# Optimization experiments

Hardware: AMD Instinct MI355X
Metric: run time of the kernel (lower is better)

## Reference

```python
import math
import jax, jax.numpy as jnp
import numpy as np

B, N, M = 8, 1024, 32
D = 128      # node_dim
E = 32       # edge_dim
DD = 32      # dist_dim
MSG = 128    # message_dim
P = 128      # proj_dim
THETA = 10000.0


def _linear(x, w, b):
    return x @ w + b


def _sinusoidal(t, dim, theta=THETA):
    half = dim // 2
    freqs = jnp.exp(jnp.arange(half, dtype=t.dtype) * (-math.log(theta) / (half - 1)))
    ang = t[..., None] * freqs  # (..., half)
    return jnp.concatenate([jnp.sin(ang), jnp.cos(ang)], axis=-1)


def setup_inputs() -> dict:
    key = jax.random.key(0)
    ks = jax.random.split(key, 20)
    pair_in = 2 * D + E + DD  # NUM_ATOMS == 1

    def w(k, shape):
        fan_in = shape[0]
        return jax.random.uniform(k, shape, jnp.float32, -1, 1) / np.sqrt(fan_in)

    return {
        "embeddings": jax.random.normal(ks[0], (B, N, D), jnp.float32),
        "coords": jax.random.normal(ks[1], (B, N, 3), jnp.float32),
        "padding_mask": jnp.ones((B, N), jnp.float32),
        "edges": jax.random.normal(ks[2], (B, N, M, E), jnp.float32),
        "we_w1": w(ks[3], (pair_in, MSG)), "we_b1": jnp.zeros((MSG,), jnp.float32),
        "we_w2": w(ks[4], (MSG, MSG)),    "we_b2": jnp.zeros((MSG,), jnp.float32),
        "wx_w1": w(ks[5], (MSG, P)),      "wx_b1": jnp.zeros((P,), jnp.float32),
        "wx_w2": w(ks[6], (P, 1)),        "wx_b2": jnp.zeros((1,), jnp.float32),
        "wh_w1": w(ks[7], (D + MSG, P)),  "wh_b1": jnp.zeros((P,), jnp.float32),
        "wh_w2": w(ks[8], (P, D)),        "wh_b2": jnp.zeros((D,), jnp.float32),
        "neighbor_ids": jax.random.randint(ks[9], (B, N, M), 0, N),
    }


def _gather(x, idx):
    # x: (B, N, d), idx: (B, N, M) -> (B, N, M, d). Direct gather,
    # mathematically identical to the one-hot einsum in the original.
    Bx, Nx, d = x.shape
    flat = jnp.take_along_axis(x, idx.reshape(Bx, -1, 1), axis=1)
    return flat.reshape(Bx, Nx, idx.shape[-1], d)


def reference(embeddings, coords, padding_mask, edges,
              we_w1, we_b1, we_w2, we_b2,
              wx_w1, wx_b1, wx_w2, wx_b2,
              wh_w1, wh_b1, wh_w2, wh_b2,
              neighbor_ids):
    feats2 = _gather(embeddings, neighbor_ids)          # (B,N,M,D)
    n_coords = _gather(coords, neighbor_ids)            # (B,N,M,3)
    rel_coors = coords[:, :, None, :] - n_coords        # (B,N,M,3)
    rel_dist = jnp.linalg.norm(rel_coors, axis=-1)      # (B,N,M)
    dists = _sinusoidal(rel_dist, DD)                   # (B,N,M,DD)

    feats1 = jnp.broadcast_to(embeddings[:, :, None, :], feats2.shape)
    feats_pair = jnp.concatenate([feats1, feats2, dists, edges], axis=-1)

    h = jax.nn.relu(_linear(feats_pair, we_w1, we_b1))
    m_ij = _linear(h, we_w2, we_b2)                     # (B,N,M,MSG)

    # coordinate update (unit vectors are detached in the original)
    unit = jax.lax.stop_gradient(
        jnp.nan_to_num(rel_coors / rel_dist[..., None]))
    px = _linear(jax.nn.relu(_linear(m_ij, wx_w1, wx_b1)), wx_w2, wx_b2)
    coords_out = coords + (unit * px).sum(axis=2) / M

    # feature update
    m_masked = m_ij * padding_mask[:, :, None, None]
    m_i = m_masked.sum(axis=2) / M                      # (B,N,MSG)
    hh = jnp.concatenate([embeddings, m_i], axis=-1)
    ph = _linear(jax.nn.relu(_linear(hh, wh_w1, wh_b1)), wh_w2, wh_b2)
    embeddings_out = embeddings + ph

    return embeddings_out, coords_out
```

## Files before the change

kernel.cpp:

```cpp
#include <hip/hip_runtime.h>
#include <hip/hip_bf16.h>

typedef __hip_bfloat16 bf16;
typedef short short8 __attribute__((ext_vector_type(8)));
typedef float f32x4 __attribute__((ext_vector_type(4)));
typedef int   int4v __attribute__((ext_vector_type(4)));

#define NB 8
#define NN 1024
#define NM 32
#define ND 128
#define NE 32
#define NODES (NB*NN)
#define NPB 4
#define NR  (NPB*NM)

#define OFF_W1AT   0
#define OFF_W1BT   32768
#define OFF_W1CDT  65536
#define OFF_W2T    81920
#define OFF_WX1T   114688
#define OFF_WH1AT  147456
#define OFF_WH1BT  180224
#define OFF_WH2T   212992
#define OFF_Y1     245760
#define OFF_Y2     (OFF_Y1 + 2097152)
#define NEED_FAST  ((size_t)OFF_Y2 + 2097152)

__device__ __forceinline__ float toF(bf16 x){ return __bfloat162float(x); }
__device__ __forceinline__ bf16  toB(float x){ return __float2bfloat16(x); }

__device__ __forceinline__ void bar_lds(){
  asm volatile("s_waitcnt lgkmcnt(0)" ::: "memory");
  __builtin_amdgcn_s_barrier();
}

__device__ __forceinline__ short8 pin8(short8 w){
  union { short8 s; int4v i; } u; u.s = w;
  asm volatile("" : "+v"(u.i));
  return u.s;
}

__device__ __forceinline__ void cp16f(bf16* d, const float* s){
  #pragma unroll
  for (int q = 0; q < 4; ++q){
    float4 a = ((const float4*)s)[q];
    d[q*4+0]=toB(a.x); d[q*4+1]=toB(a.y); d[q*4+2]=toB(a.z); d[q*4+3]=toB(a.w);
  }
}
__device__ __forceinline__ void cp8f(bf16* d, const float* s){
  #pragma unroll
  for (int q = 0; q < 2; ++q){
    float4 a = ((const float4*)s)[q];
    d[q*4+0]=toB(a.x); d[q*4+1]=toB(a.y); d[q*4+2]=toB(a.z); d[q*4+3]=toB(a.w);
  }
}
__device__ __forceinline__ void cp4f(bf16* d, const float* s){
  float4 a = *(const float4*)s;
  d[0]=toB(a.x); d[1]=toB(a.y); d[2]=toB(a.z); d[3]=toB(a.w);
}

#define MFMA(a,b,c) __builtin_amdgcn_mfma_f32_16x16x32_bf16((a),(b),(c),0,0,0)

__global__ __launch_bounds__(256) void k_tr(const float* __restrict__ w1,
    const float* __restrict__ w2, const float* __restrict__ wx1,
    const float* __restrict__ wh1, const float* __restrict__ wh2,
    char* __restrict__ ws){
  int i = blockIdx.x*256 + threadIdx.x;
  const float* src; int koff, KT, dst, e;
  if      (i <  16384){ src=w1;  koff=0;   KT=128; dst=OFF_W1AT;  e=i; }
  else if (i <  32768){ src=w1;  koff=128; KT=128; dst=OFF_W1BT;  e=i-16384; }
  else if (i <  40960){ src=w1;  koff=256; KT=64;  dst=OFF_W1CDT; e=i-32768; }
  else if (i <  57344){ src=w2;  koff=0;   KT=128; dst=OFF_W2T;   e=i-40960; }
  else if (i <  73728){ src=wx1; koff=0;   KT=128; dst=OFF_WX1T;  e=i-57344; }
  else if (i <  90112){ src=wh1; koff=0;   KT=128; dst=OFF_WH1AT; e=i-73728; }
  else if (i < 106496){ src=wh1; koff=128; KT=128; dst=OFF_WH1BT; e=i-90112; }
  else if (i < 122880){ src=wh2; koff=0;   KT=128; dst=OFF_WH2T;  e=i-106496; }
  else return;
  int c = e / KT, k = e - c*KT;
  ((bf16*)(ws+dst))[e] = toB(src[(size_t)(koff+k)*128 + c]);
}

__global__ __launch_bounds__(256) void k_prep(const float* __restrict__ emb,
    const float* __restrict__ eb1, char* __restrict__ ws){
  __shared__ __align__(16) bf16 sE[32][136];
  const int tid = threadIdx.x, g0 = blockIdx.x*32;
  { const int row = tid >> 3, sub = tid & 7;
    cp16f(&sE[row][sub*16], emb + (size_t)(g0+row)*ND + sub*16); }
  bar_lds();
  const int lane = tid & 63, wv = tid >> 6, lr = lane & 15, lk = lane >> 4;
  const int c0 = wv*16 + lr, c1 = (wv+4)*16 + lr;
  const short* wt[2] = {(const short*)(ws+OFF_W1AT), (const short*)(ws+OFF_W1BT)};
  bf16* yo[2] = {(bf16*)(ws+OFF_Y1), (bf16*)(ws+OFF_Y2)};
  #pragma unroll
  for (int t = 0; t < 2; ++t){
    f32x4 acc[2][2] = {};
    #pragma unroll
    for (int kc = 0; kc < 4; ++kc){
      const int k0 = kc*32 + lk*8;
      short8 a0 = *(const short8*)&sE[lr][k0];
      short8 a1 = *(const short8*)&sE[16+lr][k0];
      short8 w0 = *(const short8*)&wt[t][c0*128 + k0];
      short8 w1v= *(const short8*)&wt[t][c1*128 + k0];
      acc[0][0]=MFMA(a0,w0,acc[0][0]);  acc[1][0]=MFMA(a1,w0,acc[1][0]);
      acc[0][1]=MFMA(a0,w1v,acc[0][1]); acc[1][1]=MFMA(a1,w1v,acc[1][1]);
    }
    const float b0 = (t==0) ? eb1[c0] : 0.f;
    const float b1 = (t==0) ? eb1[c1] : 0.f;
    #pragma unroll
    for (int rt = 0; rt < 2; ++rt)
      #pragma unroll
      for (int r = 0; r < 4; ++r){
        const int orow = rt*16 + lk*4 + r;
        const size_t g = (size_t)(g0 + orow)*ND;
        yo[t][g + c0] = toB(acc[rt][0][r] + b0);
        yo[t][g + c1] = toB(acc[rt][1][r] + b1);
      }
  }
}

__global__ __launch_bounds__(512) void k_edges_fast(
    const float* __restrict__ coords, const float* __restrict__ mask,
    const float* __restrict__ edges,  const float* __restrict__ eb2,
    const float* __restrict__ xb1,    const float* __restrict__ xw2,
    const float* __restrict__ xb2,    const int* __restrict__ nids,
    const char* __restrict__ ws,      float* __restrict__ out)
{
  const short* w1cdT = (const short*)(ws+OFF_W1CDT);
  const short* w2T   = (const short*)(ws+OFF_W2T);
  const short* wx1T  = (const short*)(ws+OFF_WX1T);
  const bf16*  Y1    = (const bf16*)(ws+OFF_Y1);
  const bf16*  Y2    = (const bf16*)(ws+OFF_Y2);

  __shared__ __align__(16) char regA[NR*136*2];
  __shared__ __align__(16) bf16 sH[NR][136];
  __shared__ float sUnit[NR][3];
  __shared__ float sPx[NR];
  bf16 (*sDE)[72]  = (bf16(*)[72])regA;
  bf16 (*sM)[136]  = (bf16(*)[136])regA;

  const int bid = blockIdx.x;
  const int nbk = ((bid & 7) << 8) + (bid >> 3);
  const int g0  = nbk * NPB;
  const int bi  = g0 >> 10;
  const int tid = threadIdx.x;
  const int lane = tid & 63, wv = tid >> 6;
  const int lr = lane & 15, lk = lane >> 4;
  const int c0 = wv*16 + lr;

  short8 rw1[2], rw2[4], rwx[4];
  #pragma unroll
  for (int kc = 0; kc < 2; ++kc)
    rw1[kc] = pin8(*(const short8*)&w1cdT[c0*64 + kc*32 + lk*8]);
  #pragma unroll
  for (int kc = 0; kc < 4; ++kc){
    rw2[kc] = pin8(*(const short8*)&w2T[c0*128 + kc*32 + lk*8]);
    rwx[kc] = pin8(*(const short8*)&wx1T[c0*128 + kc*32 + lk*8]);
  }
  const float b2   = eb2[c0];
  const float bx   = xb1[c0];
  const float wx2c = xw2[c0];
  const float bx2v = xb2[0];
  float mv[NPB];
  #pragma unroll
  for (int n = 0; n < NPB; ++n) mv[n] = mask[g0+n];

  {
    const int row = tid >> 2, sub = tid & 3;
    const int node = row >> 5;
    const int j = nids[(size_t)(g0+node)*NM + (row & 31)];
    const float* cs = coords + (size_t)(g0+node)*3;
    const float* cj = coords + ((size_t)bi*NN + j)*3;
    const float rx = cs[0]-cj[0], ry = cs[1]-cj[1], rz = cs[2]-cj[2];
    const float d2 = rx*rx + ry*ry + rz*rz;
    const float dist = sqrtf(d2);
    if (sub == 0){
      const float inv = (d2 > 0.f) ? 1.f/dist : 0.f;
      sUnit[row][0]=rx*inv; sUnit[row][1]=ry*inv; sUnit[row][2]=rz*inv;
    }
    cp8f(&sDE[row][32 + sub*8],
         edges + ((size_t)(g0+node)*NM + (row&31))*NE + sub*8);
    #pragma unroll
    for (int q = 0; q < 8; ++q){
      const int dd = sub*8 + q, h = dd & 15;
      const float ang = dist * __expf(-0.6140226909f * (float)h);
      sDE[row][dd] = toB((dd < 16) ? __sinf(ang) : __cosf(ang));
    }
    const bf16* y1p = Y1 + (size_t)(g0+node)*ND + sub*32;
    const bf16* y2p = Y2 + ((size_t)bi*NN + j)*ND + sub*32;
    #pragma unroll
    for (int h8 = 0; h8 < 4; ++h8){
      short8 a = *(const short8*)(y1p + h8*8);
      short8 b = *(const short8*)(y2p + h8*8);
      short8 o;
      #pragma unroll
      for (int q = 0; q < 8; ++q){
        bf16 ba, bb; short sa = a[q], sb = b[q];
        __builtin_memcpy(&ba,&sa,2); __builtin_memcpy(&bb,&sb,2);
        bf16 rsum = toB(toF(ba) + toF(bb));
        short sr; __builtin_memcpy(&sr,&rsum,2);
        o[q] = sr;
      }
      *(short8*)&sH[row][sub*32 + h8*8] = o;
    }
  }
  bar_lds();

  {
    #pragma unroll
    for (int t = 0; t < 8; ++t){
      f32x4 acc = {};
      #pragma unroll
      for (int kc = 0; kc < 2; ++kc){
        short8 a = *(const short8*)&sDE[t*16 + lr][kc*32 + lk*8];
        acc = MFMA(a, rw1[kc], acc);
      }
      #pragma unroll
      for (int r = 0; r < 4; ++r){
        const int orow = t*16 + lk*4 + r;
        sH[orow][c0] = toB(fmaxf(toF(sH[orow][c0]) + acc[r], 0.f));
      }
    }
  }
  bar_lds();

  {
    float msum[NPB] = {};
    #pragma unroll
    for (int t = 0; t < 8; ++t){
      f32x4 acc = {};
      #pragma unroll
      for (int kc = 0; kc < 4; ++kc){
        short8 a = *(const short8*)&sH[t*16 + lr][kc*32 + lk*8];
        acc = MFMA(a, rw2[kc], acc);
      }
      #pragma unroll
      for (int r = 0; r < 4; ++r){
        const int orow = t*16 + lk*4 + r;
        const float m = acc[r] + b2;
        sM[orow][c0] = toB(m);
        msum[t>>1] += m;
      }
    }
    #pragma unroll
    for (int n = 0; n < NPB; ++n){
      msum[n] += __shfl_xor(msum[n], 16);
      msum[n] += __shfl_xor(msum[n], 32);
    }
    if (lk == 0){
      #pragma unroll
      for (int n = 0; n < NPB; ++n)
        out[(size_t)(g0+n)*ND + c0] = msum[n] * mv[n] * (1.f/32.f);
    }
  }
  bar_lds();

  {
    #pragma unroll
    for (int t = 0; t < 8; ++t){
      f32x4 acc = {};
      #pragma unroll
      for (int kc = 0; kc < 4; ++kc){
        short8 a = *(const short8*)&sM[t*16 + lr][kc*32 + lk*8];
        acc = MFMA(a, rwx[kc], acc);
      }
      #pragma unroll
      for (int r = 0; r < 4; ++r){
        const int orow = t*16 + lk*4 + r;
        sH[orow][c0] = toB(fmaxf(acc[r] + bx, 0.f) * wx2c);
      }
    }
  }
  bar_lds();

  {
    const int row = tid >> 2, sub = tid & 3;
    float p = 0.f;
    #pragma unroll
    for (int c8 = 0; c8 < 4; ++c8){
      short8 x = *(const short8*)&sH[row][sub*32 + c8*8];
      #pragma unroll
      for (int q = 0; q < 8; ++q){
        bf16 bq; short sq = x[q]; __builtin_memcpy(&bq,&sq,2);
        p += toF(bq);
      }
    }
    p += __shfl_xor(p, 1); p += __shfl_xor(p, 2);
    if (sub == 0) sPx[row] = p + bx2v;
  }
  bar_lds();

  if (tid < NR){
    const float px = sPx[tid];
    float v0 = sUnit[tid][0]*px, v1 = sUnit[tid][1]*px, v2 = sUnit[tid][2]*px;
    #pragma unroll
    for (int m = 1; m < 32; m <<= 1){
      v0 += __shfl_xor(v0, m);
      v1 += __shfl_xor(v1, m);
      v2 += __shfl_xor(v2, m);
    }
    const int node = tid >> 5, d = tid & 31;
    if (d < 3){
      const float s = (d==0) ? v0 : (d==1 ? v1 : v2);
      out[(size_t)NODES*ND + (size_t)(g0+node)*3 + d] =
          coords[(size_t)(g0+node)*3 + d] + s*(1.f/32.f);
    }
  }
}

__global__ __launch_bounds__(256) void k_edges_compact(
    const float* __restrict__ emb,   const float* __restrict__ coords,
    const float* __restrict__ mask,  const float* __restrict__ edges,
    const float* __restrict__ eb1,   const float* __restrict__ eb2,
    const float* __restrict__ xb1,   const float* __restrict__ xw2,
    const float* __restrict__ xb2,   const int* __restrict__ nids,
    const char* __restrict__ ws,     float* __restrict__ out)
{
  const short* w1aT  = (const short*)(ws+OFF_W1AT);
  const short* w1bT  = (const short*)(ws+OFF_W1BT);
  const short* w1cdT = (const short*)(ws+OFF_W1CDT);
  const short* w2T   = (const short*)(ws+OFF_W2T);
  const short* wx1T  = (const short*)(ws+OFF_WX1T);

  __shared__ __align__(16) bf16 sA[32][336];
  __shared__ __align__(16) bf16 sH[32][136];
  __shared__ __align__(16) bf16 sM[32][136];
  __shared__ float sUnit[32][3];
  __shared__ float sPx[32];
  __shared__ int   sIds[32];
  __shared__ float sSelfC[3];

  const int tid = threadIdx.x;
  const int nb  = blockIdx.x;
  const int bi  = nb >> 10;

  if (tid < 32) sIds[tid] = nids[nb*NM + tid];
  if (tid < 3)  sSelfC[tid] = coords[(size_t)nb*3 + tid];
  __syncthreads();

  {
    const int row = tid >> 3, sub = tid & 7;
    const int j = sIds[row];
    cp16f(&sA[row][sub*16],       emb + (size_t)nb*ND + sub*16);
    cp16f(&sA[row][128 + sub*16], emb + ((size_t)bi*NN + j)*ND + sub*16);
    cp4f (&sA[row][288 + sub*4],  edges + ((size_t)nb*NM + row)*NE + sub*4);
    float jx = coords[((size_t)bi*NN + j)*3 + 0];
    float jy = coords[((size_t)bi*NN + j)*3 + 1];
    float jz = coords[((size_t)bi*NN + j)*3 + 2];
    float rx = sSelfC[0]-jx, ry = sSelfC[1]-jy, rz = sSelfC[2]-jz;
    float d2 = rx*rx + ry*ry + rz*rz;
    float dist = sqrtf(d2);
    if (sub == 0){
      float inv = (d2 > 0.f) ? 1.f/dist : 0.f;
      sUnit[row][0]=rx*inv; sUnit[row][1]=ry*inv; sUnit[row][2]=rz*inv;
    }
    #pragma unroll
    for (int q = 0; q < 4; ++q){
      const int dd = sub*4 + q, h = dd & 15;
      float ang = dist * __expf(-0.6140226909f * (float)h);
      sA[row][256+dd] = toB((dd < 16) ? __sinf(ang) : __cosf(ang));
    }
  }
  __syncthreads();

  const int lane = tid & 63, wv = tid >> 6, lr = lane & 15, lk = lane >> 4;
  const int c0 = wv*16 + lr, c1 = (wv+4)*16 + lr;

  {
    f32x4 acc[2][2] = {};
    #pragma unroll
    for (int kc = 0; kc < 10; ++kc){
      const int k0 = kc*32 + lk*8;
      const short* wp; int kk, KT;
      if (kc < 4){ wp = w1aT; kk = k0; KT = 128; }
      else if (kc < 8){ wp = w1bT; kk = k0-128; KT = 128; }
      else { wp = w1cdT; kk = k0-256; KT = 64; }
      short8 a0 = *(const short8*)&sA[lr][k0];
      short8 a1 = *(const short8*)&sA[16+lr][k0];
      short8 w0 = *(const short8*)&wp[c0*KT + kk];
      short8 w1v= *(const short8*)&wp[c1*KT + kk];
      acc[0][0]=MFMA(a0,w0,acc[0][0]);  acc[1][0]=MFMA(a1,w0,acc[1][0]);
      acc[0][1]=MFMA(a0,w1v,acc[0][1]); acc[1][1]=MFMA(a1,w1v,acc[1][1]);
    }
    const float b0 = eb1[c0], b1 = eb1[c1];
    #pragma unroll
    for (int rt = 0; rt < 2; ++rt)
      #pragma unroll
      for (int r = 0; r < 4; ++r){
        const int orow = rt*16 + lk*4 + r;
        sH[orow][c0] = toB(fmaxf(acc[rt][0][r]+b0, 0.f));
        sH[orow][c1] = toB(fmaxf(acc[rt][1][r]+b1, 0.f));
      }
  }
  __syncthreads();

  {
    f32x4 acc[2][2] = {};
    #pragma unroll
    for (int kc = 0; kc < 4; ++kc){
      const int k0 = kc*32 + lk*8;
      short8 a0 = *(const short8*)&sH[lr][k0];
      short8 a1 = *(const short8*)&sH[16+lr][k0];
      short8 w0 = *(const short8*)&w2T[c0*128 + k0];
      short8 w1v= *(const short8*)&w2T[c1*128 + k0];
      acc[0][0]=MFMA(a0,w0,acc[0][0]);  acc[1][0]=MFMA(a1,w0,acc[1][0]);
      acc[0][1]=MFMA(a0,w1v,acc[0][1]); acc[1][1]=MFMA(a1,w1v,acc[1][1]);
    }
    const float b0 = eb2[c0], b1 = eb2[c1];
    #pragma unroll
    for (int rt = 0; rt < 2; ++rt)
      #pragma unroll
      for (int r = 0; r < 4; ++r){
        const int orow = rt*16 + lk*4 + r;
        sM[orow][c0] = toB(acc[rt][0][r] + b0);
        sM[orow][c1] = toB(acc[rt][1][r] + b1);
      }
  }
  __syncthreads();

  {
    f32x4 acc[2][2] = {};
    #pragma unroll
    for (int kc = 0; kc < 4; ++kc){
      const int k0 = kc*32 + lk*8;
      short8 a0 = *(const short8*)&sM[lr][k0];
      short8 a1 = *(const short8*)&sM[16+lr][k0];
      short8 w0 = *(const short8*)&wx1T[c0*128 + k0];
      short8 w1v= *(const short8*)&wx1T[c1*128 + k0];
      acc[0][0]=MFMA(a0,w0,acc[0][0]);  acc[1][0]=MFMA(a1,w0,acc[1][0]);
      acc[0][1]=MFMA(a0,w1v,acc[0][1]); acc[1][1]=MFMA(a1,w1v,acc[1][1]);
    }
    const float b0 = xb1[c0], b1 = xb1[c1];
    #pragma unroll
    for (int rt = 0; rt < 2; ++rt)
      #pragma unroll
      for (int r = 0; r < 4; ++r){
        const int orow = rt*16 + lk*4 + r;
        sH[orow][c0] = toB(fmaxf(acc[rt][0][r]+b0, 0.f));
        sH[orow][c1] = toB(fmaxf(acc[rt][1][r]+b1, 0.f));
      }
  }
  __syncthreads();

  {
    const int row = tid >> 3, sub = tid & 7;
    float p = 0.f;
    #pragma unroll
    for (int q = 0; q < 16; ++q){
      const int c = sub*16 + q;
      p += toF(sH[row][c]) * xw2[c];
    }
    p += __shfl_down(p,4,8); p += __shfl_down(p,2,8); p += __shfl_down(p,1,8);
    if (sub == 0) sPx[row] = p + xb2[0];
  }
  if (tid < 128){
    float s = 0.f;
    #pragma unroll
    for (int m = 0; m < 32; ++m) s += toF(sM[m][tid]);
    out[(size_t)nb*ND + tid] = s * mask[nb] * (1.f/32.f);
  }
  __syncthreads();
  if (tid < 3){
    float s = 0.f;
    #pragma unroll
    for (int m = 0; m < 32; ++m) s += sUnit[m][tid]*sPx[m];
    out[(size_t)NODES*ND + (size_t)nb*3 + tid] = sSelfC[tid] + s*(1.f/32.f);
  }
}

__global__ __launch_bounds__(256) void k_node(
    const float* __restrict__ emb, const float* __restrict__ hb1,
    const float* __restrict__ hb2, const char* __restrict__ ws,
    float* __restrict__ out)
{
  const short* whaT = (const short*)(ws+OFF_WH1AT);
  const short* whbT = (const short*)(ws+OFF_WH1BT);
  const short* wh2T = (const short*)(ws+OFF_WH2T);
  __shared__ __align__(16) bf16 sE[32][136];
  __shared__ __align__(16) bf16 sM[32][136];
  __shared__ __align__(16) bf16 sH[32][136];
  const int tid = threadIdx.x, g0 = blockIdx.x*32;
  const int lane = tid & 63, wv = tid >> 6, lr = lane & 15, lk = lane >> 4;
  const int c0 = wv*16 + lr, c1 = (wv+4)*16 + lr;

  short8 rwa[2][4], rwb[2][4], rw2[2][4];
  #pragma unroll
  for (int kc = 0; kc < 4; ++kc){
    rwa[0][kc] = *(const short8*)&whaT[c0*128 + kc*32 + lk*8];
    rwa[1][kc] = *(const short8*)&whaT[c1*128 + kc*32 + lk*8];
    rwb[0][kc] = *(const short8*)&whbT[c0*128 + kc*32 + lk*8];
    rwb[1][kc] = *(const short8*)&whbT[c1*128 + kc*32 + lk*8];
    rw2[0][kc] = *(const short8*)&wh2T[c0*128 + kc*32 + lk*8];
    rw2[1][kc] = *(const short8*)&wh2T[c1*128 + kc*32 + lk*8];
  }
  const float b1c0 = hb1[c0], b1c1 = hb1[c1];
  const float b2c0 = hb2[c0], b2c1 = hb2[c1];

  { const int row = tid >> 3, sub = tid & 7;
    cp16f(&sE[row][sub*16], emb + (size_t)(g0+row)*ND + sub*16);
    cp16f(&sM[row][sub*16], out + (size_t)(g0+row)*ND + sub*16); }
  bar_lds();
  {
    f32x4 acc[2][2] = {};
    #pragma unroll
    for (int kc = 0; kc < 4; ++kc){
      const int k0 = kc*32 + lk*8;
      short8 a0 = *(const short8*)&sE[lr][k0];
      short8 a1 = *(const short8*)&sE[16+lr][k0];
      acc[0][0]=MFMA(a0,rwa[0][kc],acc[0][0]); acc[1][0]=MFMA(a1,rwa[0][kc],acc[1][0]);
      acc[0][1]=MFMA(a0,rwa[1][kc],acc[0][1]); acc[1][1]=MFMA(a1,rwa[1][kc],acc[1][1]);
    }
    #pragma unroll
    for (int kc = 0; kc < 4; ++kc){
      const int k0 = kc*32 + lk*8;
      short8 a0 = *(const short8*)&sM[lr][k0];
      short8 a1 = *(const short8*)&sM[16+lr][k0];
      acc[0][0]=MFMA(a0,rwb[0][kc],acc[0][0]); acc[1][0]=MFMA(a1,rwb[0][kc],acc[1][0]);
      acc[0][1]=MFMA(a0,rwb[1][kc],acc[0][1]); acc[1][1]=MFMA(a1,rwb[1][kc],acc[1][1]);
    }
    #pragma unroll
    for (int rt = 0; rt < 2; ++rt)
      #pragma unroll
      for (int r = 0; r < 4; ++r){
        const int orow = rt*16 + lk*4 + r;
        sH[orow][c0] = toB(fmaxf(acc[rt][0][r] + b1c0, 0.f));
        sH[orow][c1] = toB(fmaxf(acc[rt][1][r] + b1c1, 0.f));
      }
  }
  bar_lds();
  {
    f32x4 acc[2][2] = {};
    #pragma unroll
    for (int kc = 0; kc < 4; ++kc){
      const int k0 = kc*32 + lk*8;
      short8 a0 = *(const short8*)&sH[lr][k0];
      short8 a1 = *(const short8*)&sH[16+lr][k0];
      acc[0][0]=MFMA(a0,rw2[0][kc],acc[0][0]); acc[1][0]=MFMA(a1,rw2[0][kc],acc[1][0]);
      acc[0][1]=MFMA(a0,rw2[1][kc],acc[0][1]); acc[1][1]=MFMA(a1,rw2[1][kc],acc[1][1]);
    }
    #pragma unroll
    for (int rt = 0; rt < 2; ++rt)
      #pragma unroll
      for (int r = 0; r < 4; ++r){
        const int orow = rt*16 + lk*4 + r;
        const size_t g = (size_t)(g0 + orow)*ND;
        out[g + c0] = acc[rt][0][r] + b2c0 + emb[g + c0];
        out[g + c1] = acc[rt][1][r] + b2c1 + emb[g + c1];
      }
  }
}

extern "C" void kernel_launch(void* const* d_in, const int* in_sizes, int n_in,
                              void* d_out, int out_size, void* d_ws, size_t ws_size,
                              hipStream_t stream) {
  const float* emb    = (const float*)d_in[0];
  const float* coords = (const float*)d_in[1];
  const float* mask   = (const float*)d_in[2];
  const float* edges  = (const float*)d_in[3];
  const float* we_w1  = (const float*)d_in[4];
  const float* we_b1  = (const float*)d_in[5];
  const float* we_w2  = (const float*)d_in[6];
  const float* we_b2  = (const float*)d_in[7];
  const float* wx_w1  = (const float*)d_in[8];
  const float* wx_b1  = (const float*)d_in[9];
  const float* wx_w2  = (const float*)d_in[10];
  const float* wx_b2  = (const float*)d_in[11];
  const float* wh_w1  = (const float*)d_in[12];
  const float* wh_b1  = (const float*)d_in[13];
  const float* wh_w2  = (const float*)d_in[14];
  const float* wh_b2  = (const float*)d_in[15];
  const int*   nids   = (const int*)d_in[16];
  float* out = (float*)d_out;
  char* ws = (char*)d_ws;
  const bool fast = (ws_size >= NEED_FAST);

  k_tr<<<480,256,0,stream>>>(we_w1, we_w2, wx_w1, wh_w1, wh_w2, ws);

  if (fast){
    k_prep<<<NODES/32,256,0,stream>>>(emb, we_b1, ws);
    k_edges_fast<<<NODES/NPB,512,0,stream>>>(coords, mask, edges, we_b2,
        wx_b1, wx_w2, wx_b2, nids, ws, out);
  } else {
    k_edges_compact<<<NODES,256,0,stream>>>(emb, coords, mask, edges,
        we_b1, we_b2, wx_b1, wx_w2, wx_b2, nids, ws, out);
  }

  k_node<<<NODES/32,256,0,stream>>>(emb, wh_b1, wh_b2, ws, out);
}
```

Measured before the change: 72.43 us.

## Fold second edge linear layer into downstream weights to skip one edge GEMM

Precomputes W2·Wx1 and W2·Wh1b (plus folded biases) in a new compose kernel, so the edge kernel goes straight from the hidden activation h to the coordinate-MLP preactivation and writes the mean of h instead of m. The node kernel then uses the composed weight and adds a mask-scaled folded bias. This removes one 128x128 MFMA GEMM per edge tile, one LDS round trip and one barrier. In exchange it adds a small serial compose launch and changes the bf16 rounding points.

```diff
diff --git a/kernel.cpp b/kernel.cpp
--- a/kernel.cpp
+++ b/kernel.cpp
@@ -23,7 +23,11 @@
 #define OFF_WH1AT  147456
 #define OFF_WH1BT  180224
 #define OFF_WH2T   212992
-#define OFF_Y1     245760
+#define OFF_W2XT   245760
+#define OFF_W2HT   278528
+#define OFF_B2X    311296
+#define OFF_B2H    311808
+#define OFF_Y1     312320
 #define OFF_Y2     (OFF_Y1 + 2097152)
 #define NEED_FAST  ((size_t)OFF_Y2 + 2097152)
 
@@ -81,6 +85,30 @@
   ((bf16*)(ws+dst))[e] = toB(src[(size_t)(koff+k)*128 + c]);
 }
 
+__global__ __launch_bounds__(128) void k_compose(const float* __restrict__ w2,
+    const float* __restrict__ wx1, const float* __restrict__ wh1,
+    const float* __restrict__ b2, const float* __restrict__ bx1,
+    char* __restrict__ ws){
+  const int c = blockIdx.x, k = threadIdx.x;
+  float sx = 0.f, sh = 0.f;
+  for (int q = 0; q < 128; ++q){
+    const float w2kq = w2[k*128 + q];
+    sx += w2kq * wx1[q*128 + c];
+    sh += w2kq * wh1[(128+q)*128 + c];
+  }
+  ((bf16*)(ws+OFF_W2XT))[c*128 + k] = toB(sx);
+  ((bf16*)(ws+OFF_W2HT))[c*128 + k] = toB(sh);
+  if (k == 0){
+    float bx = 0.f, bh = 0.f;
+    for (int q = 0; q < 128; ++q){
+      bx += b2[q] * wx1[q*128 + c];
+      bh += b2[q] * wh1[(128+q)*128 + c];
+    }
+    ((float*)(ws+OFF_B2X))[c] = bx + bx1[c];
+    ((float*)(ws+OFF_B2H))[c] = bh;
+  }
+}
+
 __global__ __launch_bounds__(256) void k_prep(const float* __restrict__ emb,
     const float* __restrict__ eb1, char* __restrict__ ws){
   __shared__ __align__(16) bf16 sE[32][136];
@@ -121,23 +149,22 @@
 
 __global__ __launch_bounds__(512) void k_edges_fast(
     const float* __restrict__ coords, const float* __restrict__ mask,
-    const float* __restrict__ edges,  const float* __restrict__ eb2,
-    const float* __restrict__ xb1,    const float* __restrict__ xw2,
+    const float* __restrict__ edges,  const float* __restrict__ xw2,
     const float* __restrict__ xb2,    const int* __restrict__ nids,
     const char* __restrict__ ws,      float* __restrict__ out)
 {
   const short* w1cdT = (const short*)(ws+OFF_W1CDT);
-  const short* w2T   = (const short*)(ws+OFF_W2T);
-  const short* wx1T  = (const short*)(ws+OFF_WX1T);
+  const short* w2xT  = (const short*)(ws+OFF_W2XT);
   const bf16*  Y1    = (const bf16*)(ws+OFF_Y1);
   const bf16*  Y2    = (const bf16*)(ws+OFF_Y2);
+  const float* B2X   = (const float*)(ws+OFF_B2X);
 
   __shared__ __align__(16) char regA[NR*136*2];
   __shared__ __align__(16) bf16 sH[NR][136];
   __shared__ float sUnit[NR][3];
   __shared__ float sPx[NR];
   bf16 (*sDE)[72]  = (bf16(*)[72])regA;
-  bf16 (*sM)[136]  = (bf16(*)[136])regA;
+  bf16 (*sX)[136]  = (bf16(*)[136])regA;
 
   const int bid = blockIdx.x;
   const int nbk = ((bid & 7) << 8) + (bid >> 3);
@@ -148,18 +175,15 @@
   const int lr = lane & 15, lk = lane >> 4;
   const int c0 = wv*16 + lr;
 
-  short8 rw1[2], rw2[4], rwx[4];
+  short8 rw1[2], rwx[4];
   #pragma unroll
   for (int kc = 0; kc < 2; ++kc)
     rw1[kc] = pin8(*(const short8*)&w1cdT[c0*64 + kc*32 + lk*8]);
   #pragma unroll
-  for (int kc = 0; kc < 4; ++kc){
-    rw2[kc] = pin8(*(const short8*)&w2T[c0*128 + kc*32 + lk*8]);
-    rwx[kc] = pin8(*(const short8*)&wx1T[c0*128 + kc*32 + lk*8]);
-  }
-  const float b2   = eb2[c0];
-  const float bx   = xb1[c0];
-  const float wx2c = xw2[c0];
+  for (int kc = 0; kc < 4; ++kc)
+    rwx[kc] = pin8(*(const short8*)&w2xT[c0*128 + kc*32 + lk*8]);
+  const float bxc  = B2X[c0];
+  const float wxc  = xw2[c0];
   const float bx2v = xb2[0];
   float mv[NPB];
   #pragma unroll
@@ -207,6 +231,7 @@
   bar_lds();
 
   {
+    float hsum[NPB] = {};
     #pragma unroll
     for (int t = 0; t < 8; ++t){
       f32x4 acc = {};
@@ -218,56 +243,37 @@
       #pragma unroll
       for (int r = 0; r < 4; ++r){
         const int orow = t*16 + lk*4 + r;
-        sH[orow][c0] = toB(fmaxf(toF(sH[orow][c0]) + acc[r], 0.f));
-      }
+        const float hv = fmaxf(toF(sH[orow][c0]) + acc[r], 0.f);
+        sH[orow][c0] = toB(hv);
+        hsum[t>>1] += hv;
+      }
+    }
+    #pragma unroll
+    for (int n = 0; n < NPB; ++n){
+      hsum[n] += __shfl_xor(hsum[n], 16);
+      hsum[n] += __shfl_xor(hsum[n], 32);
+    }
+    if (lk == 0){
+      #pragma unroll
+      for (int n = 0; n < NPB; ++n)
+        out[(size_t)(g0+n)*ND + c0] = hsum[n] * mv[n] * (1.f/32.f);
     }
   }
   bar_lds();
 
   {
-    float msum[NPB] = {};
     #pragma unroll
     for (int t = 0; t < 8; ++t){
       f32x4 acc = {};
       #pragma unroll
       for (int kc = 0; kc < 4; ++kc){
         short8 a = *(const short8*)&sH[t*16 + lr][kc*32 + lk*8];
-        acc = MFMA(a, rw2[kc], acc);
+        acc = MFMA(a, rwx[kc], acc);
       }
       #pragma unroll
       for (int r = 0; r < 4; ++r){
         const int orow = t*16 + lk*4 + r;
-        const float m = acc[r] + b2;
-        sM[orow][c0] = toB(m);
-        msum[t>>1] += m;
-      }
-    }
-    #pragma unroll
-    for (int n = 0; n < NPB; ++n){
-      msum[n] += __shfl_xor(msum[n], 16);
-      msum[n] += __shfl_xor(msum[n], 32);
-    }
-    if (lk == 0){
-      #pragma unroll
-      for (int n = 0; n < NPB; ++n)
-        out[(size_t)(g0+n)*ND + c0] = msum[n] * mv[n] * (1.f/32.f);
-    }
-  }
-  bar_lds();
-
-  {
-    #pragma unroll
-    for (int t = 0; t < 8; ++t){
-      f32x4 acc = {};
-      #pragma unroll
-      for (int kc = 0; kc < 4; ++kc){
-        short8 a = *(const short8*)&sM[t*16 + lr][kc*32 + lk*8];
-        acc = MFMA(a, rwx[kc], acc);
-      }
-      #pragma unroll
-      for (int r = 0; r < 4; ++r){
-        const int orow = t*16 + lk*4 + r;
-        sH[orow][c0] = toB(fmaxf(acc[r] + bx, 0.f) * wx2c);
+        sX[orow][c0] = toB(fmaxf(acc[r] + bxc, 0.f) * wxc);
       }
     }
   }
@@ -278,7 +284,7 @@
     float p = 0.f;
     #pragma unroll
     for (int c8 = 0; c8 < 4; ++c8){
-      short8 x = *(const short8*)&sH[row][sub*32 + c8*8];
+      short8 x = *(const short8*)&sX[row][sub*32 + c8*8];
       #pragma unroll
       for (int q = 0; q < 8; ++q){
         bf16 bq; short sq = x[q]; __builtin_memcpy(&bq,&sq,2);
@@ -468,17 +474,20 @@
   }
 }
 
+template<int HB>
 __global__ __launch_bounds__(256) void k_node(
-    const float* __restrict__ emb, const float* __restrict__ hb1,
-    const float* __restrict__ hb2, const char* __restrict__ ws,
-    float* __restrict__ out)
+    const float* __restrict__ emb, const float* __restrict__ mask,
+    const float* __restrict__ hb1, const float* __restrict__ hb2,
+    const char* __restrict__ ws, float* __restrict__ out)
 {
   const short* whaT = (const short*)(ws+OFF_WH1AT);
-  const short* whbT = (const short*)(ws+OFF_WH1BT);
+  const short* whbT = (const short*)(ws + (HB ? OFF_W2HT : OFF_WH1BT));
   const short* wh2T = (const short*)(ws+OFF_WH2T);
+  const float* b2h  = (const float*)(ws+OFF_B2H);
   __shared__ __align__(16) bf16 sE[32][136];
   __shared__ __align__(16) bf16 sM[32][136];
   __shared__ __align__(16) bf16 sH[32][136];
+  __shared__ float sMask[32];
   const int tid = threadIdx.x, g0 = blockIdx.x*32;
   const int lane = tid & 63, wv = tid >> 6, lr = lane & 15, lk = lane >> 4;
   const int c0 = wv*16 + lr, c1 = (wv+4)*16 + lr;
@@ -495,10 +504,13 @@
   }
   const float b1c0 = hb1[c0], b1c1 = hb1[c1];
   const float b2c0 = hb2[c0], b2c1 = hb2[c1];
+  const float bhc0 = HB ? b2h[c0] : 0.f;
+  const float bhc1 = HB ? b2h[c1] : 0.f;
 
   { const int row = tid >> 3, sub = tid & 7;
     cp16f(&sE[row][sub*16], emb + (size_t)(g0+row)*ND + sub*16);
     cp16f(&sM[row][sub*16], out + (size_t)(g0+row)*ND + sub*16); }
+  if (tid < 32) sMask[tid] = mask[g0 + tid];
   bar_lds();
   {
     f32x4 acc[2][2] = {};
@@ -523,8 +535,9 @@
       #pragma unroll
       for (int r = 0; r < 4; ++r){
         const int orow = rt*16 + lk*4 + r;
-        sH[orow][c0] = toB(fmaxf(acc[rt][0][r] + b1c0, 0.f));
-        sH[orow][c1] = toB(fmaxf(acc[rt][1][r] + b1c1, 0.f));
+        const float mk = HB ? sMask[orow] : 0.f;
+        sH[orow][c0] = toB(fmaxf(acc[rt][0][r] + b1c0 + mk*bhc0, 0.f));
+        sH[orow][c1] = toB(fmaxf(acc[rt][1][r] + b1c1 + mk*bhc1, 0.f));
       }
   }
   bar_lds();
@@ -577,13 +590,14 @@
   k_tr<<<480,256,0,stream>>>(we_w1, we_w2, wx_w1, wh_w1, wh_w2, ws);
 
   if (fast){
+    k_compose<<<128,128,0,stream>>>(we_w2, wx_w1, wh_w1, we_b2, wx_b1, ws);
     k_prep<<<NODES/32,256,0,stream>>>(emb, we_b1, ws);
-    k_edges_fast<<<NODES/NPB,512,0,stream>>>(coords, mask, edges, we_b2,
-        wx_b1, wx_w2, wx_b2, nids, ws, out);
+    k_edges_fast<<<NODES/NPB,512,0,stream>>>(coords, mask, edges,
+        wx_w2, wx_b2, nids, ws, out);
+    k_node<1><<<NODES/32,256,0,stream>>>(emb, mask, wh_b1, wh_b2, ws, out);
   } else {
     k_edges_compact<<<NODES,256,0,stream>>>(emb, coords, mask, edges,
         we_b1, we_b2, wx_b1, wx_w2, wx_b2, nids, ws, out);
-  }
-
-  k_node<<<NODES/32,256,0,stream>>>(emb, wh_b1, wh_b2, ws, out);
-}
+    k_node<0><<<NODES/32,256,0,stream>>>(emb, mask, wh_b1, wh_b2, ws, out);
+  }
+}
```

Result: slower. 77.69 us (+7.3%).
